# Kernel optimization log

Hardware: AMD Instinct MI355X
Metric: run time of the kernel (lower is better)

The kernel has to match this reference:

```python
import jax, jax.numpy as jnp
import numpy as np

PATTERN_BOOST = 1.2


def setup_inputs() -> dict:
    key = jax.random.key(0)
    k1, k2 = jax.random.split(key)
    B, S, L = 64, 8192, 24
    logits = jax.random.normal(k1, (B, S, L), dtype=jnp.float32)
    labels = jax.random.randint(k2, (B, S, L), 0, 2).astype(jnp.int32)  # binary multi-label targets
    attention_mask = jnp.ones((B, S), dtype=jnp.float32)
    return {"logits": logits, "labels": labels, "attention_mask": attention_mask}


def reference(logits, labels, attention_mask):
    y = labels.astype(logits.dtype)
    # numerically-stable BCE-with-logits, elementwise (reduction='none')
    loss = jnp.maximum(logits, 0) - logits * y + jnp.log1p(jnp.exp(-jnp.abs(logits)))
    # vectorized pattern boost: positions i in [0, S-2] where step i and i+1 both have any punct
    has_punct = labels.sum(axis=-1) > 0                      # [B, S]
    pair = has_punct[:, :-1] & has_punct[:, 1:]              # [B, S-1]
    boost = 1.0 + pair.astype(logits.dtype) * (PATTERN_BOOST - 1.0)
    boost = jnp.pad(boost, ((0, 0), (0, 1)), constant_values=1.0)  # last timestep never boosted
    loss = loss * boost[:, :, None]
    mask = attention_mask[:, :, None].astype(logits.dtype)   # [B, S, 1]
    return (loss * mask).sum() / mask.sum()
```

## Files before the change

kernel.cpp:

```cpp
#include <hip/hip_runtime.h>

constexpr int Bdim = 64;
constexpr int S = 8192;
constexpr int L = 24;
constexpr int NPOS = Bdim * S;
constexpr int POS_PER_BLK = 128;
constexpr int NBLK = NPOS / POS_PER_BLK;
constexpr int BLK_PER_ROW = S / POS_PER_BLK;
constexpr float BOOST = 1.2f;

__device__ __forceinline__ float bce(float x, float y) {
    float e = __expf(-fabsf(x));
    float l = __logf(1.0f + e);
    return fmaxf(x, 0.0f) - x * y + l;
}

__global__ __launch_bounds__(256) void pal_main(
    const float* __restrict__ logits,
    const int*   __restrict__ labels,
    const float* __restrict__ mask,
    double*      __restrict__ partials)
{
    __shared__ float psum[768];
    __shared__ float plab[768];
    __shared__ unsigned char hp_next_sh;
    __shared__ float wl[4], wm[4];

    const int t = threadIdx.x;
    const size_t cbase = (size_t)blockIdx.x * 768;

    if (t == 0) {
        int hn = 0;
        if ((blockIdx.x & (BLK_PER_ROW - 1)) != BLK_PER_ROW - 1) {
            const int4* nb = (const int4*)labels + cbase + 768;
            int sn = 0;
#pragma unroll
            for (int j = 0; j < 6; ++j) { int4 v = nb[j]; sn += v.x + v.y + v.z + v.w; }
            hn = (sn > 0) ? 1 : 0;
        }
        hp_next_sh = (unsigned char)hn;
    }

#pragma unroll
    for (int k = 0; k < 3; ++k) {
        const size_t c = cbase + (size_t)t + 256 * k;
        float4 lg = ((const float4*)logits)[c];
        int4   lb = ((const int4*)labels)[c];
        float s = 0.0f;
        s += bce(lg.x, (float)lb.x);
        s += bce(lg.y, (float)lb.y);
        s += bce(lg.z, (float)lb.z);
        s += bce(lg.w, (float)lb.w);
        psum[t + 256 * k] = s;
        plab[t + 256 * k] = (float)(lb.x + lb.y + lb.z + lb.w);
    }
    __syncthreads();

    float contrib = 0.0f, m = 0.0f;
    if (t < POS_PER_BLK) {
        float ls = 0.0f, lab = 0.0f;
#pragma unroll
        for (int j = 0; j < 6; ++j) { ls += psum[6 * t + j]; lab += plab[6 * t + j]; }
        int hp = (lab > 0.0f);
        int hpn;
        if (t < POS_PER_BLK - 1) {
            float ln = 0.0f;
#pragma unroll
            for (int j = 0; j < 6; ++j) ln += plab[6 * t + 6 + j];
            hpn = (ln > 0.0f);
        } else {
            hpn = hp_next_sh;
        }
        float boost = (hp && hpn) ? BOOST : 1.0f;
        m = mask[(size_t)blockIdx.x * POS_PER_BLK + t];
        contrib = ls * boost * m;
    }

#pragma unroll
    for (int off = 32; off > 0; off >>= 1) {
        contrib += __shfl_down(contrib, off, 64);
        m       += __shfl_down(m, off, 64);
    }
    if ((t & 63) == 0) { wl[t >> 6] = contrib; wm[t >> 6] = m; }
    __syncthreads();
    if (t == 0) {
        double Ls = (double)wl[0] + (double)wl[1] + (double)wl[2] + (double)wl[3];
        double Ms = (double)wm[0] + (double)wm[1] + (double)wm[2] + (double)wm[3];
        partials[2 * blockIdx.x]     = Ls;
        partials[2 * blockIdx.x + 1] = Ms;
    }
}

__global__ __launch_bounds__(256) void pal_final(
    const double* __restrict__ partials,
    float*        __restrict__ out)
{
    const int t = threadIdx.x;
    double l = 0.0, m = 0.0;
    for (int i = t; i < NBLK; i += 256) {
        l += partials[2 * i];
        m += partials[2 * i + 1];
    }
    __shared__ double sl[256], sm[256];
    sl[t] = l; sm[t] = m;
    __syncthreads();
    for (int off = 128; off > 0; off >>= 1) {
        if (t < off) { sl[t] += sl[t + off]; sm[t] += sm[t + off]; }
        __syncthreads();
    }
    if (t == 0) out[0] = (float)(sl[0] / sm[0]);
}

extern "C" void kernel_launch(void* const* d_in, const int* in_sizes, int n_in,
                              void* d_out, int out_size, void* d_ws, size_t ws_size,
                              hipStream_t stream) {
    const float* logits = (const float*)d_in[0];
    const int*   labels = (const int*)d_in[1];
    const float* mask   = (const float*)d_in[2];
    float*  out = (float*)d_out;
    double* partials = (double*)d_ws;

    pal_main <<<NBLK, 256, 0, stream>>>(logits, labels, mask, partials);
    pal_final<<<1,    256, 0, stream>>>(partials, out);
}
```

Measured before the change: 122.4 us.

## Fuse final reduction via last-block atomic counter and double positions per block

Each block now handles 256 positions instead of 128, which halves the block count and uses all threads in the per-position phase. The separate final-reduction kernel is replaced by an atomic counter, so the last block to finish sums the partials in the same launch. A memset of the counter is added to the stream in place of the second kernel launch. The cost is an atomic and a fence per block, plus more shared memory per block, which may reduce occupancy.

```diff
diff --git a/kernel.cpp b/kernel.cpp
--- a/kernel.cpp
+++ b/kernel.cpp
@@ -4,7 +4,7 @@
 constexpr int S = 8192;
 constexpr int L = 24;
 constexpr int NPOS = Bdim * S;
-constexpr int POS_PER_BLK = 128;
+constexpr int POS_PER_BLK = 256;
 constexpr int NBLK = NPOS / POS_PER_BLK;
 constexpr int BLK_PER_ROW = S / POS_PER_BLK;
 constexpr float BOOST = 1.2f;
@@ -19,20 +19,23 @@
     const float* __restrict__ logits,
     const int*   __restrict__ labels,
     const float* __restrict__ mask,
-    double*      __restrict__ partials)
+    double*       __restrict__ partials,
+    unsigned int* __restrict__ counter,
+    float*        __restrict__ out)
 {
-    __shared__ float psum[768];
-    __shared__ float plab[768];
+    __shared__ float psum[1536];
+    __shared__ float plab[1536];
     __shared__ unsigned char hp_next_sh;
     __shared__ float wl[4], wm[4];
+    __shared__ int   is_last_sh;
 
     const int t = threadIdx.x;
-    const size_t cbase = (size_t)blockIdx.x * 768;
+    const size_t cbase = (size_t)blockIdx.x * 1536;
 
     if (t == 0) {
         int hn = 0;
         if ((blockIdx.x & (BLK_PER_ROW - 1)) != BLK_PER_ROW - 1) {
-            const int4* nb = (const int4*)labels + cbase + 768;
+            const int4* nb = (const int4*)labels + cbase + 1536;
             int sn = 0;
 #pragma unroll
             for (int j = 0; j < 6; ++j) { int4 v = nb[j]; sn += v.x + v.y + v.z + v.w; }
@@ -42,7 +45,7 @@
     }
 
 #pragma unroll
-    for (int k = 0; k < 3; ++k) {
+    for (int k = 0; k < 6; ++k) {
         const size_t c = cbase + (size_t)t + 256 * k;
         float4 lg = ((const float4*)logits)[c];
         int4   lb = ((const int4*)labels)[c];
@@ -56,25 +59,22 @@
     }
     __syncthreads();
 
-    float contrib = 0.0f, m = 0.0f;
-    if (t < POS_PER_BLK) {
-        float ls = 0.0f, lab = 0.0f;
+    float ls = 0.0f, lab = 0.0f;
 #pragma unroll
-        for (int j = 0; j < 6; ++j) { ls += psum[6 * t + j]; lab += plab[6 * t + j]; }
-        int hp = (lab > 0.0f);
-        int hpn;
-        if (t < POS_PER_BLK - 1) {
-            float ln = 0.0f;
+    for (int j = 0; j < 6; ++j) { ls += psum[6 * t + j]; lab += plab[6 * t + j]; }
+    const int hp = (lab > 0.0f);
+    int hpn;
+    if (t < POS_PER_BLK - 1) {
+        float ln = 0.0f;
 #pragma unroll
-            for (int j = 0; j < 6; ++j) ln += plab[6 * t + 6 + j];
-            hpn = (ln > 0.0f);
-        } else {
-            hpn = hp_next_sh;
-        }
-        float boost = (hp && hpn) ? BOOST : 1.0f;
-        m = mask[(size_t)blockIdx.x * POS_PER_BLK + t];
-        contrib = ls * boost * m;
+        for (int j = 0; j < 6; ++j) ln += plab[6 * t + 6 + j];
+        hpn = (ln > 0.0f);
+    } else {
+        hpn = hp_next_sh;
     }
+    const float boost = (hp && hpn) ? BOOST : 1.0f;
+    float m = mask[(size_t)blockIdx.x * POS_PER_BLK + t];
+    float contrib = ls * boost * m;
 
 #pragma unroll
     for (int off = 32; off > 0; off >>= 1) {
@@ -83,32 +83,36 @@
     }
     if ((t & 63) == 0) { wl[t >> 6] = contrib; wm[t >> 6] = m; }
     __syncthreads();
+
     if (t == 0) {
         double Ls = (double)wl[0] + (double)wl[1] + (double)wl[2] + (double)wl[3];
         double Ms = (double)wm[0] + (double)wm[1] + (double)wm[2] + (double)wm[3];
         partials[2 * blockIdx.x]     = Ls;
         partials[2 * blockIdx.x + 1] = Ms;
+        __threadfence();
+        unsigned int prev = __hip_atomic_fetch_add(counter, 1u,
+                                __ATOMIC_ACQ_REL, __HIP_MEMORY_SCOPE_AGENT);
+        is_last_sh = (prev == NBLK - 1);
     }
-}
+    __syncthreads();
 
-__global__ __launch_bounds__(256) void pal_final(
-    const double* __restrict__ partials,
-    float*        __restrict__ out)
-{
-    const int t = threadIdx.x;
-    double l = 0.0, m = 0.0;
-    for (int i = t; i < NBLK; i += 256) {
-        l += partials[2 * i];
-        m += partials[2 * i + 1];
+    if (is_last_sh) {
+        double l = 0.0, mm = 0.0;
+        for (int i = t; i < NBLK; i += 256) {
+            l  += __hip_atomic_load(&partials[2 * i],     __ATOMIC_RELAXED,
+                                    __HIP_MEMORY_SCOPE_AGENT);
+            mm += __hip_atomic_load(&partials[2 * i + 1], __ATOMIC_RELAXED,
+                                    __HIP_MEMORY_SCOPE_AGENT);
+        }
+        __shared__ double sl[256], sm[256];
+        sl[t] = l; sm[t] = mm;
+        __syncthreads();
+        for (int off = 128; off > 0; off >>= 1) {
+            if (t < off) { sl[t] += sl[t + off]; sm[t] += sm[t + off]; }
+            __syncthreads();
+        }
+        if (t == 0) out[0] = (float)(sl[0] / sm[0]);
     }
-    __shared__ double sl[256], sm[256];
-    sl[t] = l; sm[t] = m;
-    __syncthreads();
-    for (int off = 128; off > 0; off >>= 1) {
-        if (t < off) { sl[t] += sl[t + off]; sm[t] += sm[t + off]; }
-        __syncthreads();
-    }
-    if (t == 0) out[0] = (float)(sl[0] / sm[0]);
 }
 
 extern "C" void kernel_launch(void* const* d_in, const int* in_sizes, int n_in,
@@ -117,9 +121,11 @@
     const float* logits = (const float*)d_in[0];
     const int*   labels = (const int*)d_in[1];
     const float* mask   = (const float*)d_in[2];
-    float*  out = (float*)d_out;
-    double* partials = (double*)d_ws;
+    float* out = (float*)d_out;
 
-    pal_main <<<NBLK, 256, 0, stream>>>(logits, labels, mask, partials);
-    pal_final<<<1,    256, 0, stream>>>(partials, out);
+    double*       partials = (double*)d_ws;
+    unsigned int* counter  = (unsigned int*)((char*)d_ws + 2 * NBLK * sizeof(double));
+
+    hipMemsetAsync(counter, 0, sizeof(unsigned int), stream);
+    pal_main<<<NBLK, 256, 0, stream>>>(logits, labels, mask, partials, counter, out);
 }
```

Result: slower. 229.5 us (+87.4%).
